# Performance work log

Measured on AMD Instinct MI355X. Metric: run time of the kernel, lower is better.

## Reference

```python
import jax, jax.numpy as jnp
import numpy as np

BOARD = 19
N_ORBITS = 55

def build_bias_map():
    # Reproduce the exact (quirky) torch init loop, including re-assignment of
    # the 0-valued orbit: cells whose value stays 0 get overwritten by later counters.
    m = np.zeros((BOARD, BOARD), dtype=np.int64)
    counter = 0
    for i in range(BOARD):
        for j in range(BOARD):
            if m[i, j] != 0:
                continue
            for a, b in ((i, j), (18 - i, j), (i, 18 - j), (18 - i, 18 - j),
                         (j, i), (j, 18 - i), (18 - j, i), (18 - j, 18 - i)):
                m[a, b] = counter
            counter += 1
    # torch does bias[biasMap - 1]; value 0 -> index -1 (wraps to last element)
    return (m - 1) % N_ORBITS  # [19,19] int

def setup_inputs() -> dict:
    key = jax.random.key(0)
    k1, k2, k3 = jax.random.split(key, 3)
    x = jax.random.normal(k1, (1024, 256, BOARD, BOARD), dtype=jnp.float32)
    conv_w = jax.random.normal(k2, (1, 256, 1, 1), dtype=jnp.float32) * 0.05
    bias = jax.random.normal(k3, (N_ORBITS,), dtype=jnp.float32) * 0.05
    return {"x": x, "conv_w": conv_w, "bias": bias}

def reference(x, conv_w, bias):
    # 1x1 conv, out_channels=1, no bias: contraction over channel dim
    w = conv_w[0, :, 0, 0]                       # [C]
    y = jnp.einsum('bchw,c->bhw', x, w)          # [B,19,19]
    idx = jnp.asarray(build_bias_map())          # [19,19] static constant
    y = y + bias[idx]                            # fused gather-add over spatial
    return y.reshape(y.shape[0], -1)             # flatten -> [B,361]
```

## Files before the change

### kernel.cpp

```cpp
#include <hip/hip_runtime.h>

#define BOARD 19
#define HW    361
#define NC    256
#define CHUNK 32
#define NTH   384
#define F4_PER_CHUNK ((CHUNK * HW) / 4)

__global__ __launch_bounds__(NTH)
void output_layer_kernel(const float* __restrict__ x,
                         const float* __restrict__ w,
                         const float* __restrict__ bias,
                         float* __restrict__ out)
{
    __shared__ float4 lds4[F4_PER_CHUNK];
    __shared__ float  wsh[NC];
    float* lds = reinterpret_cast<float*>(lds4);

    const int b = blockIdx.x;
    const int t = threadIdx.x;

    if (t < NC) wsh[t] = w[t];

    const float4* xb = reinterpret_cast<const float4*>(x) + (size_t)b * (NC * HW / 4);

    float acc = 0.0f;
    for (int c0 = 0; c0 < NC; c0 += CHUNK) {
        const float4* src = xb + (c0 * HW) / 4;
        #pragma unroll
        for (int i = 0; i < 8; ++i) {
            int k = t + i * NTH;
            if (k < F4_PER_CHUNK) lds4[k] = src[k];
        }
        __syncthreads();
        if (t < HW) {
            #pragma unroll
            for (int cc = 0; cc < CHUNK; ++cc)
                acc = fmaf(lds[cc * HW + t], wsh[c0 + cc], acc);
        }
        __syncthreads();
    }

    if (t < HW) {
        const int i = t / BOARD;
        const int j = t % BOARD;
        const int a  = min(i, 18 - i);
        const int bq = min(j, 18 - j);
        const int r  = min(a, bq);
        const int c  = max(a, bq);
        int counter;
        if (r == 0) counter = (c == 0) ? 10 : c;
        else        counter = 11 + (r - 1) * 10 - (r * (r - 1)) / 2 + (c - r);
        const int idx = (counter - 1) % 55;

        out[(size_t)b * HW + t] = acc + bias[idx];
    }
}

extern "C" void kernel_launch(void* const* d_in, const int* in_sizes, int n_in,
                              void* d_out, int out_size, void* d_ws, size_t ws_size,
                              hipStream_t stream)
{
    const float* x    = (const float*)d_in[0];
    const float* w    = (const float*)d_in[1];
    const float* bias = (const float*)d_in[2];
    float*       out  = (float*)d_out;

    const int B = in_sizes[0] / (NC * HW);
    hipLaunchKernelGGL(output_layer_kernel, dim3(B), dim3(NTH), 0, stream,
                       x, w, bias, out);
}
```

Baseline: 78.49 us.

## Replace LDS-staged per-batch reduction with flat per-output-thread direct loads

Drops the shared-memory staging of channel chunks and the per-chunk barriers. Instead each thread owns one output element and streams its 256 channel values straight from global memory, reading weights from global/cache and using four independent accumulators. This gives more blocks, fewer idle threads (the old kernel left 23 of 384 threads idle) and no synchronisation. In exchange each load is a scalar 4-byte access strided by 361 floats per channel rather than a float4, and coalescing across a wavefront depends on neighbouring threads reading consecutive hw positions.

```diff
diff --git a/kernel.cpp b/kernel.cpp
--- a/kernel.cpp
+++ b/kernel.cpp
@@ -3,58 +3,48 @@
 #define BOARD 19
 #define HW    361
 #define NC    256
-#define CHUNK 32
-#define NTH   384
-#define F4_PER_CHUNK ((CHUNK * HW) / 4)
+#define NTH   256
 
 __global__ __launch_bounds__(NTH)
 void output_layer_kernel(const float* __restrict__ x,
                          const float* __restrict__ w,
                          const float* __restrict__ bias,
-                         float* __restrict__ out)
+                         float* __restrict__ out,
+                         int total)
 {
-    __shared__ float4 lds4[F4_PER_CHUNK];
-    __shared__ float  wsh[NC];
-    float* lds = reinterpret_cast<float*>(lds4);
+    const int tid = blockIdx.x * NTH + threadIdx.x;
+    if (tid >= total) return;
 
-    const int b = blockIdx.x;
-    const int t = threadIdx.x;
+    const int b  = tid / HW;
+    const int hw = tid - b * HW;
 
-    if (t < NC) wsh[t] = w[t];
+    const float* __restrict__ xp = x + (size_t)b * (NC * HW) + hw;
 
-    const float4* xb = reinterpret_cast<const float4*>(x) + (size_t)b * (NC * HW / 4);
+    float a0 = 0.f, a1 = 0.f, a2 = 0.f, a3 = 0.f;
+    #pragma unroll 4
+    for (int c = 0; c < NC; c += 16) {
+        #pragma unroll
+        for (int u = 0; u < 16; u += 4) {
+            a0 = fmaf(xp[(c + u + 0) * HW], w[c + u + 0], a0);
+            a1 = fmaf(xp[(c + u + 1) * HW], w[c + u + 1], a1);
+            a2 = fmaf(xp[(c + u + 2) * HW], w[c + u + 2], a2);
+            a3 = fmaf(xp[(c + u + 3) * HW], w[c + u + 3], a3);
+        }
+    }
+    const float acc = (a0 + a1) + (a2 + a3);
 
-    float acc = 0.0f;
-    for (int c0 = 0; c0 < NC; c0 += CHUNK) {
-        const float4* src = xb + (c0 * HW) / 4;
-        #pragma unroll
-        for (int i = 0; i < 8; ++i) {
-            int k = t + i * NTH;
-            if (k < F4_PER_CHUNK) lds4[k] = src[k];
-        }
-        __syncthreads();
-        if (t < HW) {
-            #pragma unroll
-            for (int cc = 0; cc < CHUNK; ++cc)
-                acc = fmaf(lds[cc * HW + t], wsh[c0 + cc], acc);
-        }
-        __syncthreads();
-    }
+    const int i  = hw / BOARD;
+    const int j  = hw - i * BOARD;
+    const int aq = min(i, 18 - i);
+    const int bq = min(j, 18 - j);
+    const int r  = min(aq, bq);
+    const int cq = max(aq, bq);
+    int counter;
+    if (r == 0) counter = (cq == 0) ? 10 : cq;
+    else        counter = 11 + (r - 1) * 10 - (r * (r - 1)) / 2 + (cq - r);
+    const int idx = (counter - 1) % 55;
 
-    if (t < HW) {
-        const int i = t / BOARD;
-        const int j = t % BOARD;
-        const int a  = min(i, 18 - i);
-        const int bq = min(j, 18 - j);
-        const int r  = min(a, bq);
-        const int c  = max(a, bq);
-        int counter;
-        if (r == 0) counter = (c == 0) ? 10 : c;
-        else        counter = 11 + (r - 1) * 10 - (r * (r - 1)) / 2 + (c - r);
-        const int idx = (counter - 1) % 55;
-
-        out[(size_t)b * HW + t] = acc + bias[idx];
-    }
+    out[tid] = acc + bias[idx];
 }
 
 extern "C" void kernel_launch(void* const* d_in, const int* in_sizes, int n_in,
@@ -66,7 +56,8 @@
     const float* bias = (const float*)d_in[2];
     float*       out  = (float*)d_out;
 
-    const int B = in_sizes[0] / (NC * HW);
-    hipLaunchKernelGGL(output_layer_kernel, dim3(B), dim3(NTH), 0, stream,
-                       x, w, bias, out);
+    const int total  = out_size;
+    const int blocks = (total + NTH - 1) / NTH;
+    hipLaunchKernelGGL(output_layer_kernel, dim3(blocks), dim3(NTH), 0, stream,
+                       x, w, bias, out, total);
 }
```

New measurement: 73.69 us. -6.1%, faster.

## Stream x directly into registers with float4 loads, removing LDS staging

Applied to the files above, without the earlier changes.

Drops the per-chunk LDS staging of x and its two barriers per chunk. Each of the 361 active threads now reads one float4 per group of four channels straight from global memory. Because 4*361 floats span four channel planes, each float4 lane can straddle two channels, so the right weight is picked per lane and partial sums go into a small LDS buffer that is reduced across four planes at the end. This removes the LDS round trip and the synchronisation, but leaves 23 of the 384 threads idle and keeps only 64 sequential loads in flight per thread, so memory-level parallelism may be limited.

```diff
diff --git a/kernel.cpp b/kernel.cpp
--- a/kernel.cpp
+++ b/kernel.cpp
@@ -3,9 +3,8 @@
 #define BOARD 19
 #define HW    361
 #define NC    256
-#define CHUNK 32
 #define NTH   384
-#define F4_PER_CHUNK ((CHUNK * HW) / 4)
+#define NITER (NC / 4)
 
 __global__ __launch_bounds__(NTH)
 void output_layer_kernel(const float* __restrict__ x,
@@ -13,41 +12,51 @@
                          const float* __restrict__ bias,
                          float* __restrict__ out)
 {
-    __shared__ float4 lds4[F4_PER_CHUNK];
-    __shared__ float  wsh[NC];
-    float* lds = reinterpret_cast<float*>(lds4);
+    __shared__ float4 wsh4[NC / 4];
+    __shared__ float  red[4 * HW];
 
     const int b = blockIdx.x;
     const int t = threadIdx.x;
 
-    if (t < NC) wsh[t] = w[t];
-
-    const float4* xb = reinterpret_cast<const float4*>(x) + (size_t)b * (NC * HW / 4);
-
-    float acc = 0.0f;
-    for (int c0 = 0; c0 < NC; c0 += CHUNK) {
-        const float4* src = xb + (c0 * HW) / 4;
-        #pragma unroll
-        for (int i = 0; i < 8; ++i) {
-            int k = t + i * NTH;
-            if (k < F4_PER_CHUNK) lds4[k] = src[k];
-        }
-        __syncthreads();
-        if (t < HW) {
-            #pragma unroll
-            for (int cc = 0; cc < CHUNK; ++cc)
-                acc = fmaf(lds[cc * HW + t], wsh[c0 + cc], acc);
-        }
-        __syncthreads();
-    }
+    if (t < NC) reinterpret_cast<float*>(wsh4)[t] = w[t];
+    __syncthreads();
 
     if (t < HW) {
-        const int i = t / BOARD;
-        const int j = t % BOARD;
-        const int a  = min(i, 18 - i);
+        const int s  = t;
+        const int f0 = 4 * s;
+        const int c0 = f0 / HW;
+        const int c1 = (c0 < 3) ? c0 + 1 : 3;
+        const int m  = min(4, (c0 + 1) * HW - f0);
+        const bool b1 = (1 < m), b2 = (2 < m), b3 = (3 < m);
+
+        const float4* __restrict__ xb =
+            reinterpret_cast<const float4*>(x + (size_t)b * (NC * HW)) + s;
+
+        float a0 = 0.f, a1 = 0.f, a2 = 0.f, a3 = 0.f;
+        #pragma unroll 4
+        for (int i = 0; i < NITER; ++i) {
+            const float4 xv = xb[(size_t)i * HW];
+            const float4 wv = wsh4[i];
+            const float wlo = (c0 == 0) ? wv.x : (c0 == 1) ? wv.y : (c0 == 2) ? wv.z : wv.w;
+            const float whi = (c1 == 1) ? wv.y : (c1 == 2) ? wv.z : wv.w;
+            a0 = fmaf(xv.x, wlo,            a0);
+            a1 = fmaf(xv.y, b1 ? wlo : whi, a1);
+            a2 = fmaf(xv.z, b2 ? wlo : whi, a2);
+            a3 = fmaf(xv.w, b3 ? wlo : whi, a3);
+        }
+        reinterpret_cast<float4*>(red)[s] = make_float4(a0, a1, a2, a3);
+    }
+    __syncthreads();
+
+    if (t < HW) {
+        const float acc = (red[t] + red[HW + t]) + (red[2 * HW + t] + red[3 * HW + t]);
+
+        const int i  = t / BOARD;
+        const int j  = t - i * BOARD;
+        const int aq = min(i, 18 - i);
         const int bq = min(j, 18 - j);
-        const int r  = min(a, bq);
-        const int c  = max(a, bq);
+        const int r  = min(aq, bq);
+        const int c  = max(aq, bq);
         int counter;
         if (r == 0) counter = (c == 0) ? 10 : c;
         else        counter = 11 + (r - 1) * 10 - (r * (r - 1)) / 2 + (c - r);
```

After: 69.80 us. -11.1%, faster.
